# Performance work log

Measured on AMD Instinct MI355X. Metric: run time of the kernel, lower is better.

Reference implementation:

```python
import jax, jax.numpy as jnp
import numpy as np

EPS = 1e-06

def setup_inputs() -> dict:
    key = jax.random.key(0)
    k1, k2, k3, k4 = jax.random.split(key, 4)
    B, N, H, W = 8, 8, 512, 512
    pd_rgbo = jax.random.normal(k1, (B, 4, H, W), dtype=jnp.float32)
    gt_rgbo = jax.random.normal(k2, (B, 4, H, W), dtype=jnp.float32)
    pd_mask = jax.random.randint(k3, (B, N, H, W), 0, 2, dtype=jnp.int32)
    gt_mask = jax.random.randint(k4, (B, N, H, W), 0, 2, dtype=jnp.int32)
    return {"pd_rgbo": pd_rgbo, "gt_rgbo": gt_rgbo, "pd_mask": pd_mask, "gt_mask": gt_mask}

def reference(pd_rgbo, gt_rgbo, pd_mask, gt_mask):
    # masks -> bool, derived mask combinations
    pm = pd_mask.astype(bool)            # [B,N,H,W]
    gm = gt_mask.astype(bool)
    dt = pd_rgbo.dtype
    pmf = pm.astype(dt)
    and_f = (pm & gm).astype(dt)         # logical_and
    xor_f = (pm & ~gm).astype(dt)        # xor(or, gt) == pd & ~gt
    gmf = gm.astype(dt)

    pd_rgb = pd_rgbo[:, :3]              # [B,3,H,W]
    gt_rgb = gt_rgbo[:, :3]
    pd_o = jnp.round(pd_rgbo[:, 3])      # [B,H,W]
    gt_o = jnp.round(gt_rgbo[:, 3])

    # per-pixel L2 color distance over channels: [B,H,W]
    diff_norm = jnp.linalg.norm(pd_rgb - gt_rgb, ord=2, axis=1)

    # punish: mean color distance over predicted-mask pixels (per b,n)
    sim_sum = jnp.einsum('bhw,bnhw->bn', diff_norm, pmf)
    count = jnp.sum(pmf, axis=(2, 3))
    punish = sim_sum / (count + EPS)

    # IoU from rounded opacities masked by logical masks
    inter = jnp.einsum('bhw,bnhw->bn', pd_o, and_f)
    gt_sum = jnp.einsum('bhw,bnhw->bn', gt_o, gmf)
    pd_xor_sum = jnp.einsum('bhw,bnhw->bn', pd_o, xor_f)
    iou = inter / (gt_sum + pd_xor_sum + EPS)

    # weights default to ones -> plain mean over all (b, n) pairs
    loss = jnp.mean(1.0 - iou + punish)
    return loss
```

## Files before the change

kernel.cpp:

```cpp
#include <hip/hip_runtime.h>


constexpr int Bc  = 8;
constexpr int Nc  = 8;
constexpr int HWc = 512 * 512;
constexpr int PAD = 16;
constexpr int R   = 2;
constexpr int QPB = 256 * R;
constexpr float EPSc = 1e-6f;

__device__ __forceinline__ float wave_reduce(float v) {
#pragma unroll
    for (int off = 32; off; off >>= 1) v += __shfl_xor(v, off, 64);
    return v;
}

__global__ __launch_bounds__(256, 2) void niou_partial(
    const float* __restrict__ pd, const float* __restrict__ gt,
    const int* __restrict__ pmask, const int* __restrict__ gmask,
    float* __restrict__ ws )
{
    const int b   = blockIdx.x >> 7;
    const int blk = blockIdx.x & 127;
    constexpr int HW4 = HWc / 4;

    float acc[Nc][4];
    int   wcnt[Nc];
#pragma unroll
    for (int n = 0; n < Nc; ++n) {
        wcnt[n] = 0;
#pragma unroll
        for (int q = 0; q < 4; ++q) acc[n][q] = 0.f;
    }

#pragma unroll
    for (int r = 0; r < R; ++r) {
        const int quad = blk * QPB + r * 256 + threadIdx.x;
        const size_t p = (size_t)quad * 4;

        const float4* pd4 = reinterpret_cast<const float4*>(pd + (size_t)b * 4 * HWc + p);
        const float4* gt4 = reinterpret_cast<const float4*>(gt + (size_t)b * 4 * HWc + p);
        const int4*   pm4 = reinterpret_cast<const int4*>(pmask + (size_t)b * Nc * HWc + p);
        const int4*   gm4 = reinterpret_cast<const int4*>(gmask + (size_t)b * Nc * HWc + p);

        float4 pv[4], gv[4];
        int4 pmv[Nc], gmv[Nc];
#pragma unroll
        for (int c = 0; c < 4; ++c) pv[c] = pd4[c * HW4];
#pragma unroll
        for (int c = 0; c < 4; ++c) gv[c] = gt4[c * HW4];
#pragma unroll
        for (int n = 0; n < Nc; ++n) { pmv[n] = pm4[n * HW4]; gmv[n] = gm4[n * HW4]; }
        __builtin_amdgcn_sched_barrier(0);

        float dn[4], po[4], go[4];
        {
            float dx, dy, dz;
            dx = pv[0].x - gv[0].x; dy = pv[1].x - gv[1].x; dz = pv[2].x - gv[2].x;
            dn[0] = sqrtf(dx*dx + dy*dy + dz*dz); po[0] = rintf(pv[3].x); go[0] = rintf(gv[3].x);
            dx = pv[0].y - gv[0].y; dy = pv[1].y - gv[1].y; dz = pv[2].y - gv[2].y;
            dn[1] = sqrtf(dx*dx + dy*dy + dz*dz); po[1] = rintf(pv[3].y); go[1] = rintf(gv[3].y);
            dx = pv[0].z - gv[0].z; dy = pv[1].z - gv[1].z; dz = pv[2].z - gv[2].z;
            dn[2] = sqrtf(dx*dx + dy*dy + dz*dz); po[2] = rintf(pv[3].z); go[2] = rintf(gv[3].z);
            dx = pv[0].w - gv[0].w; dy = pv[1].w - gv[1].w; dz = pv[2].w - gv[2].w;
            dn[3] = sqrtf(dx*dx + dy*dy + dz*dz); po[3] = rintf(pv[3].w); go[3] = rintf(gv[3].w);
        }

#pragma unroll
        for (int n = 0; n < Nc; ++n) {
            const int pmx[4] = {pmv[n].x, pmv[n].y, pmv[n].z, pmv[n].w};
            const int gmx[4] = {gmv[n].x, gmv[n].y, gmv[n].z, gmv[n].w};
#pragma unroll
            for (int j = 0; j < 4; ++j) {
                const bool P = pmx[j] != 0;
                const bool G = gmx[j] != 0;
                wcnt[n] += __popcll(__ballot(P));
                acc[n][0] += P ? dn[j] : 0.f;
                acc[n][1] += (P && G)  ? po[j] : 0.f;
                acc[n][2] += G ? go[j] : 0.f;
                acc[n][3] += (P && !G) ? po[j] : 0.f;
            }
        }
    }

    __shared__ float red[4][40];
    const int lane = threadIdx.x & 63;
    const int wv   = threadIdx.x >> 6;
#pragma unroll
    for (int n = 0; n < Nc; ++n) {
        const float s0 = wave_reduce(acc[n][0]);
        const float s1 = wave_reduce(acc[n][1]);
        const float s2 = wave_reduce(acc[n][2]);
        const float s3 = wave_reduce(acc[n][3]);
        if (lane == 0) {
            red[wv][n * 5 + 0] = s0;
            red[wv][n * 5 + 1] = (float)wcnt[n];
            red[wv][n * 5 + 2] = s1;
            red[wv][n * 5 + 3] = s2;
            red[wv][n * 5 + 4] = s3;
        }
    }
    __syncthreads();

    const int t = threadIdx.x;
    if (t < Nc * 5) {
        const float v = red[0][t] + red[1][t] + red[2][t] + red[3][t];
        atomicAdd(&ws[(b * 40 + t) * PAD], v);
    }
}

__global__ __launch_bounds__(64) void niou_final(
    const float* __restrict__ ws, float* __restrict__ out)
{
    const int t = threadIdx.x;
    const float* w = ws + (size_t)t * 5 * PAD;
    const float sim   = w[0 * PAD];
    const float cnt   = w[1 * PAD];
    const float inter = w[2 * PAD];
    const float gts   = w[3 * PAD];
    const float xo    = w[4 * PAD];
    const float punish = sim / (cnt + EPSc);
    const float iou    = inter / (gts + xo + EPSc);
    float term = 1.0f - iou + punish;
    term = wave_reduce(term);
    if (t == 0) out[0] = term * (1.0f / 64.0f);
}

extern "C" void kernel_launch(void* const* d_in, const int* in_sizes, int n_in,
                              void* d_out, int out_size, void* d_ws, size_t ws_size,
                              hipStream_t stream) {
    const float* pd_rgbo = (const float*)d_in[0];
    const float* gt_rgbo = (const float*)d_in[1];
    const int*   pd_mask = (const int*)d_in[2];
    const int*   gt_mask = (const int*)d_in[3];
    float* out = (float*)d_out;
    float* ws  = (float*)d_ws;

    hipMemsetAsync(ws, 0, Bc * 40 * PAD * sizeof(float), stream);
    niou_partial<<<Bc * 128, 256, 0, stream>>>(pd_rgbo, gt_rgbo, pd_mask, gt_mask, ws);
    niou_final<<<1, 64, 0, stream>>>(ws, out);
}
```

Measured before the change: 44.66 us.

## Hoist all loads for both iterations and use LDS transpose for block reduction

Issues every global load for both R iterations up front, RGBO first and then masks, so more memory requests are in flight per thread before any compute starts. Replaces the per-accumulator wave shuffle reductions (32 of them) with a 256x33 padded LDS transpose followed by a column sum. This doubles register pressure for the loaded data, which could lower occupancy under launch_bounds(256,2). It also adds about 33KB of shared memory per block.

```diff
diff --git a/kernel.cpp b/kernel.cpp
--- a/kernel.cpp
+++ b/kernel.cpp
@@ -6,23 +6,55 @@
 constexpr int HWc = 512 * 512;
 constexpr int PAD = 16;
 constexpr int R   = 2;
-constexpr int QPB = 256 * R;
 constexpr float EPSc = 1e-6f;
-
-__device__ __forceinline__ float wave_reduce(float v) {
-#pragma unroll
-    for (int off = 32; off; off >>= 1) v += __shfl_xor(v, off, 64);
-    return v;
-}
 
 __global__ __launch_bounds__(256, 2) void niou_partial(
     const float* __restrict__ pd, const float* __restrict__ gt,
     const int* __restrict__ pmask, const int* __restrict__ gmask,
     float* __restrict__ ws )
 {
-    const int b   = blockIdx.x >> 7;
-    const int blk = blockIdx.x & 127;
+    const int b    = blockIdx.x >> 7;
+    const int blk  = blockIdx.x & 127;
+    const int tid  = threadIdx.x;
     constexpr int HW4 = HWc / 4;
+    const int quad0 = blk * (256 * R) + tid;
+
+    float4 pv[R][4], gv[R][4];
+    int4   pmv[R][Nc], gmv[R][Nc];
+#pragma unroll
+    for (int r = 0; r < R; ++r) {
+        const size_t p = (size_t)(quad0 + r * 256) * 4;
+        const float4* pd4 = reinterpret_cast<const float4*>(pd + (size_t)b * 4 * HWc + p);
+        const float4* gt4 = reinterpret_cast<const float4*>(gt + (size_t)b * 4 * HWc + p);
+#pragma unroll
+        for (int c = 0; c < 4; ++c) pv[r][c] = pd4[c * HW4];
+#pragma unroll
+        for (int c = 0; c < 4; ++c) gv[r][c] = gt4[c * HW4];
+    }
+    __builtin_amdgcn_sched_barrier(0);
+#pragma unroll
+    for (int r = 0; r < R; ++r) {
+        const size_t p = (size_t)(quad0 + r * 256) * 4;
+        const int4* pm4 = reinterpret_cast<const int4*>(pmask + (size_t)b * Nc * HWc + p);
+        const int4* gm4 = reinterpret_cast<const int4*>(gmask + (size_t)b * Nc * HWc + p);
+#pragma unroll
+        for (int n = 0; n < Nc; ++n) { pmv[r][n] = pm4[n * HW4]; gmv[r][n] = gm4[n * HW4]; }
+    }
+    __builtin_amdgcn_sched_barrier(0);
+
+    float dn[R][4], po[R][4], go[R][4];
+#pragma unroll
+    for (int r = 0; r < R; ++r) {
+        float dx, dy, dz;
+        dx = pv[r][0].x - gv[r][0].x; dy = pv[r][1].x - gv[r][1].x; dz = pv[r][2].x - gv[r][2].x;
+        dn[r][0] = sqrtf(dx*dx + dy*dy + dz*dz); po[r][0] = rintf(pv[r][3].x); go[r][0] = rintf(gv[r][3].x);
+        dx = pv[r][0].y - gv[r][0].y; dy = pv[r][1].y - gv[r][1].y; dz = pv[r][2].y - gv[r][2].y;
+        dn[r][1] = sqrtf(dx*dx + dy*dy + dz*dz); po[r][1] = rintf(pv[r][3].y); go[r][1] = rintf(gv[r][3].y);
+        dx = pv[r][0].z - gv[r][0].z; dy = pv[r][1].z - gv[r][1].z; dz = pv[r][2].z - gv[r][2].z;
+        dn[r][2] = sqrtf(dx*dx + dy*dy + dz*dz); po[r][2] = rintf(pv[r][3].z); go[r][2] = rintf(gv[r][3].z);
+        dx = pv[r][0].w - gv[r][0].w; dy = pv[r][1].w - gv[r][1].w; dz = pv[r][2].w - gv[r][2].w;
+        dn[r][3] = sqrtf(dx*dx + dy*dy + dz*dz); po[r][3] = rintf(pv[r][3].w); go[r][3] = rintf(gv[r][3].w);
+    }
 
     float acc[Nc][4];
     int   wcnt[Nc];
@@ -34,78 +66,56 @@
     }
 
 #pragma unroll
-    for (int r = 0; r < R; ++r) {
-        const int quad = blk * QPB + r * 256 + threadIdx.x;
-        const size_t p = (size_t)quad * 4;
-
-        const float4* pd4 = reinterpret_cast<const float4*>(pd + (size_t)b * 4 * HWc + p);
-        const float4* gt4 = reinterpret_cast<const float4*>(gt + (size_t)b * 4 * HWc + p);
-        const int4*   pm4 = reinterpret_cast<const int4*>(pmask + (size_t)b * Nc * HWc + p);
-        const int4*   gm4 = reinterpret_cast<const int4*>(gmask + (size_t)b * Nc * HWc + p);
-
-        float4 pv[4], gv[4];
-        int4 pmv[Nc], gmv[Nc];
-#pragma unroll
-        for (int c = 0; c < 4; ++c) pv[c] = pd4[c * HW4];
-#pragma unroll
-        for (int c = 0; c < 4; ++c) gv[c] = gt4[c * HW4];
-#pragma unroll
-        for (int n = 0; n < Nc; ++n) { pmv[n] = pm4[n * HW4]; gmv[n] = gm4[n * HW4]; }
-        __builtin_amdgcn_sched_barrier(0);
-
-        float dn[4], po[4], go[4];
-        {
-            float dx, dy, dz;
-            dx = pv[0].x - gv[0].x; dy = pv[1].x - gv[1].x; dz = pv[2].x - gv[2].x;
-            dn[0] = sqrtf(dx*dx + dy*dy + dz*dz); po[0] = rintf(pv[3].x); go[0] = rintf(gv[3].x);
-            dx = pv[0].y - gv[0].y; dy = pv[1].y - gv[1].y; dz = pv[2].y - gv[2].y;
-            dn[1] = sqrtf(dx*dx + dy*dy + dz*dz); po[1] = rintf(pv[3].y); go[1] = rintf(gv[3].y);
-            dx = pv[0].z - gv[0].z; dy = pv[1].z - gv[1].z; dz = pv[2].z - gv[2].z;
-            dn[2] = sqrtf(dx*dx + dy*dy + dz*dz); po[2] = rintf(pv[3].z); go[2] = rintf(gv[3].z);
-            dx = pv[0].w - gv[0].w; dy = pv[1].w - gv[1].w; dz = pv[2].w - gv[2].w;
-            dn[3] = sqrtf(dx*dx + dy*dy + dz*dz); po[3] = rintf(pv[3].w); go[3] = rintf(gv[3].w);
-        }
-
+    for (int r = 0; r < R; ++r)
 #pragma unroll
         for (int n = 0; n < Nc; ++n) {
-            const int pmx[4] = {pmv[n].x, pmv[n].y, pmv[n].z, pmv[n].w};
-            const int gmx[4] = {gmv[n].x, gmv[n].y, gmv[n].z, gmv[n].w};
+            const int pmx[4] = {pmv[r][n].x, pmv[r][n].y, pmv[r][n].z, pmv[r][n].w};
+            const int gmx[4] = {gmv[r][n].x, gmv[r][n].y, gmv[r][n].z, gmv[r][n].w};
 #pragma unroll
             for (int j = 0; j < 4; ++j) {
                 const bool P = pmx[j] != 0;
                 const bool G = gmx[j] != 0;
                 wcnt[n] += __popcll(__ballot(P));
-                acc[n][0] += P ? dn[j] : 0.f;
-                acc[n][1] += (P && G)  ? po[j] : 0.f;
-                acc[n][2] += G ? go[j] : 0.f;
-                acc[n][3] += (P && !G) ? po[j] : 0.f;
+                acc[n][0] += P ? dn[r][j] : 0.f;
+                acc[n][1] += (P && G)  ? po[r][j] : 0.f;
+                acc[n][2] += G ? go[r][j] : 0.f;
+                acc[n][3] += (P && !G) ? po[r][j] : 0.f;
             }
         }
-    }
 
-    __shared__ float red[4][40];
-    const int lane = threadIdx.x & 63;
-    const int wv   = threadIdx.x >> 6;
+    __shared__ float tr[256][33];
+    __shared__ float part[4][32];
+    __shared__ float cpart[4][Nc];
+
+    const int wv = tid >> 6;
 #pragma unroll
-    for (int n = 0; n < Nc; ++n) {
-        const float s0 = wave_reduce(acc[n][0]);
-        const float s1 = wave_reduce(acc[n][1]);
-        const float s2 = wave_reduce(acc[n][2]);
-        const float s3 = wave_reduce(acc[n][3]);
-        if (lane == 0) {
-            red[wv][n * 5 + 0] = s0;
-            red[wv][n * 5 + 1] = (float)wcnt[n];
-            red[wv][n * 5 + 2] = s1;
-            red[wv][n * 5 + 3] = s2;
-            red[wv][n * 5 + 4] = s3;
-        }
+    for (int qi = 0; qi < 32; ++qi) tr[tid][qi] = acc[qi >> 2][qi & 3];
+    if ((tid & 63) == 0) {
+#pragma unroll
+        for (int n = 0; n < Nc; ++n) cpart[wv][n] = (float)wcnt[n];
     }
     __syncthreads();
 
-    const int t = threadIdx.x;
-    if (t < Nc * 5) {
-        const float v = red[0][t] + red[1][t] + red[2][t] + red[3][t];
-        atomicAdd(&ws[(b * 40 + t) * PAD], v);
+    {
+        const int q    = tid & 31;
+        const int half = tid >> 5;
+        float s = 0.f;
+#pragma unroll
+        for (int k = 0; k < 32; ++k) s += tr[half * 32 + k][q];
+        s += __shfl_xor(s, 32, 64);
+        if ((tid & 32) == 0) part[tid >> 6][q] = s;
+    }
+    __syncthreads();
+
+    if (tid < 32) {
+        const float v = part[0][tid] + part[1][tid] + part[2][tid] + part[3][tid];
+        const int n = tid >> 2, qq = tid & 3;
+        const int slot = n * 5 + (qq == 0 ? 0 : qq + 1);
+        atomicAdd(&ws[(b * 40 + slot) * PAD], v);
+    } else if (tid >= 64 && tid < 64 + Nc) {
+        const int n = tid - 64;
+        const float c = cpart[0][n] + cpart[1][n] + cpart[2][n] + cpart[3][n];
+        atomicAdd(&ws[(b * 40 + n * 5 + 1) * PAD], c);
     }
 }
 
@@ -122,7 +132,8 @@
     const float punish = sim / (cnt + EPSc);
     const float iou    = inter / (gts + xo + EPSc);
     float term = 1.0f - iou + punish;
-    term = wave_reduce(term);
+#pragma unroll
+    for (int off = 32; off; off >>= 1) term += __shfl_xor(term, off, 64);
     if (t == 0) out[0] = term * (1.0f / 64.0f);
 }
 
```

Result: faster. 43.51 us (-2.6%).

## Shrink blocks, replace shuffle reductions with LDS transpose, derive xor sum algebraically

Applied to the files above, without the earlier changes.

Blocks shrink to 128 threads and the grid doubles to 2048, with a launch bound of 4 blocks per CU. The end-of-block reduction now goes through a padded shared-memory transpose instead of 32 wave shuffle reductions per thread, cutting shuffle instruction count. The xor accumulator becomes the plain P-masked opacity sum, and the final kernel computes xor = sum - inter, which saves a select per element. This adds more atomics on the workspace and more shared-memory traffic, and the subtraction can change rounding slightly.

```diff
diff --git a/kernel.cpp b/kernel.cpp
--- a/kernel.cpp
+++ b/kernel.cpp
@@ -6,7 +6,8 @@
 constexpr int HWc = 512 * 512;
 constexpr int PAD = 16;
 constexpr int R   = 2;
-constexpr int QPB = 256 * R;
+constexpr int TPB = 128;
+constexpr int QPB = TPB * R;
 constexpr float EPSc = 1e-6f;
 
 __device__ __forceinline__ float wave_reduce(float v) {
@@ -15,13 +16,14 @@
     return v;
 }
 
-__global__ __launch_bounds__(256, 2) void niou_partial(
+__global__ __launch_bounds__(TPB, 4) void niou_partial(
     const float* __restrict__ pd, const float* __restrict__ gt,
     const int* __restrict__ pmask, const int* __restrict__ gmask,
     float* __restrict__ ws )
 {
-    const int b   = blockIdx.x >> 7;
-    const int blk = blockIdx.x & 127;
+    const int b   = blockIdx.x >> 8;
+    const int blk = blockIdx.x & 255;
+    const int tid = threadIdx.x;
     constexpr int HW4 = HWc / 4;
 
     float acc[Nc][4];
@@ -35,7 +37,7 @@
 
 #pragma unroll
     for (int r = 0; r < R; ++r) {
-        const int quad = blk * QPB + r * 256 + threadIdx.x;
+        const int quad = blk * QPB + r * TPB + tid;
         const size_t p = (size_t)quad * 4;
 
         const float4* pd4 = reinterpret_cast<const float4*>(pd + (size_t)b * 4 * HWc + p);
@@ -75,37 +77,48 @@
                 const bool P = pmx[j] != 0;
                 const bool G = gmx[j] != 0;
                 wcnt[n] += __popcll(__ballot(P));
+                const float s = P ? po[j] : 0.f;
                 acc[n][0] += P ? dn[j] : 0.f;
-                acc[n][1] += (P && G)  ? po[j] : 0.f;
+                acc[n][1] += G ? s     : 0.f;
                 acc[n][2] += G ? go[j] : 0.f;
-                acc[n][3] += (P && !G) ? po[j] : 0.f;
+                acc[n][3] += s;
             }
         }
     }
 
-    __shared__ float red[4][40];
-    const int lane = threadIdx.x & 63;
-    const int wv   = threadIdx.x >> 6;
+    __shared__ float tr[TPB][33];
+    __shared__ float part[2][32];
+    __shared__ float cpart[2][Nc];
+
+    const int lane = tid & 63;
+    const int wv   = tid >> 6;
 #pragma unroll
-    for (int n = 0; n < Nc; ++n) {
-        const float s0 = wave_reduce(acc[n][0]);
-        const float s1 = wave_reduce(acc[n][1]);
-        const float s2 = wave_reduce(acc[n][2]);
-        const float s3 = wave_reduce(acc[n][3]);
-        if (lane == 0) {
-            red[wv][n * 5 + 0] = s0;
-            red[wv][n * 5 + 1] = (float)wcnt[n];
-            red[wv][n * 5 + 2] = s1;
-            red[wv][n * 5 + 3] = s2;
-            red[wv][n * 5 + 4] = s3;
-        }
+    for (int qi = 0; qi < 32; ++qi) tr[tid][qi] = acc[qi >> 2][qi & 3];
+    if (lane == 0) {
+#pragma unroll
+        for (int n = 0; n < Nc; ++n) cpart[wv][n] = (float)wcnt[n];
     }
     __syncthreads();
 
-    const int t = threadIdx.x;
-    if (t < Nc * 5) {
-        const float v = red[0][t] + red[1][t] + red[2][t] + red[3][t];
-        atomicAdd(&ws[(b * 40 + t) * PAD], v);
+    {
+        const int q    = tid & 31;
+        const int half = tid >> 5;
+        float s = 0.f;
+#pragma unroll
+        for (int k = 0; k < 32; ++k) s += tr[half * 32 + k][q];
+        s += __shfl_xor(s, 32, 64);
+        if ((tid & 32) == 0) part[wv][q] = s;
+    }
+    __syncthreads();
+
+    if (tid < 32) {
+        const float v = part[0][tid] + part[1][tid];
+        const int n = tid >> 2, qq = tid & 3;
+        const int slot = n * 5 + (qq == 0 ? 0 : qq + 1);
+        atomicAdd(&ws[(b * 40 + slot) * PAD], v);
+    } else if (tid >= 64 && tid < 64 + Nc) {
+        const int n = tid - 64;
+        atomicAdd(&ws[(b * 40 + n * 5 + 1) * PAD], cpart[0][n] + cpart[1][n]);
     }
 }
 
@@ -118,11 +131,13 @@
     const float cnt   = w[1 * PAD];
     const float inter = w[2 * PAD];
     const float gts   = w[3 * PAD];
-    const float xo    = w[4 * PAD];
+    const float ssum  = w[4 * PAD];
+    const float xo    = ssum - inter;
     const float punish = sim / (cnt + EPSc);
     const float iou    = inter / (gts + xo + EPSc);
     float term = 1.0f - iou + punish;
-    term = wave_reduce(term);
+#pragma unroll
+    for (int off = 32; off; off >>= 1) term += __shfl_xor(term, off, 64);
     if (t == 0) out[0] = term * (1.0f / 64.0f);
 }
 
@@ -137,6 +152,6 @@
     float* ws  = (float*)d_ws;
 
     hipMemsetAsync(ws, 0, Bc * 40 * PAD * sizeof(float), stream);
-    niou_partial<<<Bc * 128, 256, 0, stream>>>(pd_rgbo, gt_rgbo, pd_mask, gt_mask, ws);
+    niou_partial<<<Bc * 256, TPB, 0, stream>>>(pd_rgbo, gt_rgbo, pd_mask, gt_mask, ws);
     niou_final<<<1, 64, 0, stream>>>(ws, out);
 }
```

Result: slower. 55.07 us (+23.3%).
